# Kernel optimization log

Hardware: AMD Instinct MI355X
Metric: run time of the kernel (lower is better)

The kernel has to match this reference:

```python
import jax, jax.numpy as jnp
import numpy as np

TEMPERATURE = 0.5
BN_EPS = 1e-5
L2_EPS = 1e-12

B, D_IN, D_HID, D_OUT = 4096, 192, 512, 128


def setup_inputs() -> dict:
    key = jax.random.key(0)
    ks = jax.random.split(key, 4)
    return {
        "h1": jax.random.normal(ks[0], (B, D_IN), dtype=jnp.float32),
        "h2": jax.random.normal(ks[1], (B, D_IN), dtype=jnp.float32),
        "W1": jax.random.normal(ks[2], (D_HID, D_IN), dtype=jnp.float32) * (1.0 / np.sqrt(D_IN)),
        "b1": jnp.zeros((D_HID,), dtype=jnp.float32),
        "gamma": jnp.ones((D_HID,), dtype=jnp.float32),
        "beta": jnp.zeros((D_HID,), dtype=jnp.float32),
        "W2": jax.random.normal(ks[3], (D_OUT, D_HID), dtype=jnp.float32) * (1.0 / np.sqrt(D_HID)),
        "b2": jnp.zeros((D_OUT,), dtype=jnp.float32),
    }


def _projection_head(h, W1, b1, gamma, beta, W2, b2):
    # Linear -> BatchNorm1d (training-mode batch stats) -> ReLU -> Linear
    y = h @ W1.T + b1  # (B, D_HID)
    mean = jnp.mean(y, axis=0)
    var = jnp.mean((y - mean) ** 2, axis=0)  # biased var, as torch BN uses for normalization
    y = (y - mean) * jax.lax.rsqrt(var + BN_EPS) * gamma + beta
    y = jax.nn.relu(y)
    return y @ W2.T + b2  # (B, D_OUT)


def _l2_normalize(z):
    n = jnp.sqrt(jnp.sum(z * z, axis=1, keepdims=True))
    return z / jnp.maximum(n, L2_EPS)


def reference(h1, h2, W1, b1, gamma, beta, W2, b2):
    z1 = _l2_normalize(_projection_head(h1, W1, b1, gamma, beta, W2, b2))
    z2 = _l2_normalize(_projection_head(h2, W1, b1, gamma, beta, W2, b2))

    # NT-Xent, fully vectorized (equivalent to the per-row torch loop):
    z = jnp.concatenate([z1, z2], axis=0)            # (2B, D)
    sim = (z @ z.T) / TEMPERATURE                    # (2B, 2B)
    n2 = z.shape[0]
    sim = jnp.where(jnp.eye(n2, dtype=bool), -jnp.inf, sim)
    # positive pair similarity: sim[i, i+B] and sim[i+B, i] == z1_i . z2_i / T
    pos = jnp.sum(z1 * z2, axis=1) / TEMPERATURE     # (B,)
    pos = jnp.concatenate([pos, pos])                # (2B,)
    # excluding index i from the row equals including it since diag is -inf
    lse = jax.nn.logsumexp(sim, axis=1)              # (2B,)
    loss = jnp.mean(lse - pos)
    return loss, z1, z2
```

## Files before the change

### kernel.cpp

```cpp
#include <hip/hip_runtime.h>


#define NB   4096
#define DIN  192
#define DHID 512
#define DOUT 128
#define N2   8192
#define NSPLIT 32
#define SIM_ITERS 16

typedef short short8 __attribute__((ext_vector_type(8)));
typedef float floatx4 __attribute__((ext_vector_type(4)));

__device__ inline float fast_exp2(float x) {
#if __has_builtin(__builtin_amdgcn_exp2f)
    return __builtin_amdgcn_exp2f(x);
#else
    return exp2f(x);
#endif
}

__device__ inline unsigned short bf16_rne(float x) {
    unsigned int u = __float_as_uint(x);
    return (unsigned short)((u + 0x7fffu + ((u >> 16) & 1u)) >> 16);
}

#define NW1 (DHID * DIN / 4)
#define NW2 (DOUT * DHID / 4)
#define NH  (NB * DIN / 4)
__global__ __launch_bounds__(256) void convert_w(
    const float* __restrict__ W1, const float* __restrict__ W2,
    const float* __restrict__ h1, const float* __restrict__ h2,
    unsigned short* __restrict__ W1b, unsigned short* __restrict__ W2b,
    unsigned short* __restrict__ Hb)
{
    int id = blockIdx.x * 256 + threadIdx.x;
    const float* src; unsigned short* dst; int off;
    if (id < NW1)                 { src = W1; dst = W1b; off = id; }
    else if (id < NW1 + NW2)      { src = W2; dst = W2b; off = id - NW1; }
    else if (id < NW1 + NW2 + NH) { src = h1; dst = Hb;  off = id - NW1 - NW2; }
    else if (id < NW1 + NW2 + 2 * NH) {
        src = h2; dst = Hb + (size_t)NB * DIN; off = id - NW1 - NW2 - NH;
    } else return;
    float4 x = ((const float4*)src)[off];
    unsigned int p0 = bf16_rne(x.x) | ((unsigned int)bf16_rne(x.y) << 16);
    unsigned int p1 = bf16_rne(x.z) | ((unsigned int)bf16_rne(x.w) << 16);
    ((uint2*)dst)[off] = make_uint2(p0, p1);
}

__global__ __launch_bounds__(256) void gemm1_mfma(
    const unsigned short* __restrict__ Hb,
    const unsigned short* __restrict__ W1b, const float* __restrict__ b1,
    unsigned short* __restrict__ Ybf,
    float* __restrict__ psumc, float* __restrict__ psqc)
{
    const int t = threadIdx.x;
    const int wave = t >> 6, lane = t & 63;
    const int quad = lane >> 4, l15 = lane & 15;
    const int mb = blockIdx.x;
    const int m0 = mb * 64 + wave * 16;
    const int n0 = blockIdx.y * 64;
    const int v  = (mb >= 64);

    short8 a[6];
    {
        const short8* ap = (const short8*)(Hb + (size_t)(m0 + l15) * DIN + quad * 8);
        #pragma unroll
        for (int kc = 0; kc < 6; ++kc) a[kc] = ap[kc * 4];
    }

    #pragma unroll
    for (int nt = 0; nt < 4; ++nt) {
        const int col = n0 + nt * 16 + l15;
        const short8* bptr = (const short8*)(W1b + (size_t)col * DIN + quad * 8);
        short8 b[6];
        #pragma unroll
        for (int kc = 0; kc < 6; ++kc) b[kc] = bptr[kc * 4];
        floatx4 acc = {0.f,0.f,0.f,0.f};
        #pragma unroll
        for (int kc = 0; kc < 6; ++kc)
            acc = __builtin_amdgcn_mfma_f32_16x16x32_bf16(a[kc], b[kc], acc, 0,0,0);
        const float bias = b1[col];
        float cs = 0.f, cq = 0.f;
        #pragma unroll
        for (int reg = 0; reg < 4; ++reg) {
            float y = acc[reg] + bias;
            int row = m0 + quad * 4 + reg;
            Ybf[(size_t)row * DHID + col] = bf16_rne(y);
            cs += y; cq += y * y;
        }
        cs += __shfl_xor(cs, 16); cs += __shfl_xor(cs, 32);
        cq += __shfl_xor(cq, 16); cq += __shfl_xor(cq, 32);
        if (quad == 0) {
            atomicAdd(psumc + v * DHID + col, cs);
            atomicAdd(psqc  + v * DHID + col, cq);
        }
    }
}

#define ZSCALE 1.6986436f

__global__ __launch_bounds__(512) void gemm2_mfma(
    const unsigned short* __restrict__ Ybf, const unsigned short* __restrict__ W2b,
    const float* __restrict__ psumc, const float* __restrict__ psqc,
    const float* __restrict__ gamma, const float* __restrict__ beta,
    const float* __restrict__ b2,
    unsigned short* __restrict__ Zb, float* __restrict__ outz)
{
    __shared__ float sc_sh[DHID], sh_sh[DHID];
    __shared__ float sq_lds[8][16];
    const int t = threadIdx.x;
    const int wave = t >> 6, lane = t & 63;
    const int quad = lane >> 4, l15 = lane & 15;
    const int mtbase = blockIdx.x * 16;
    const int v = (mtbase >= NB);
    const int col = wave * 16 + l15;

    {
        int c = t;
        float mean = psumc[v * DHID + c] * (1.0f / NB);
        float var  = psqc [v * DHID + c] * (1.0f / NB) - mean * mean;
        float rstd = rsqrtf(var + 1e-5f);
        float scv = gamma[c] * rstd;
        sc_sh[c] = scv;
        sh_sh[c] = beta[c] - mean * scv;
    }
    __syncthreads();

    const unsigned short* yrow = Ybf + (size_t)(mtbase + l15) * DHID + quad * 8;
    const unsigned short* wcol = W2b + (size_t)col * DHID + quad * 8;

    uint4 ycur = *(const uint4*)yrow;
    short8 bcur = *(const short8*)wcol;
    floatx4 acc = {0.f, 0.f, 0.f, 0.f};

    for (int kc = 0; kc < 16; ++kc) {
        uint4 ynext; short8 bnext;
        const int kn = (kc + 1) & 15;
        ynext = *(const uint4*)(yrow + kn * 32);
        bnext = *(const short8*)(wcol + kn * 32);

        const int k = kc * 32 + quad * 8;
        const float4 s0 = *(const float4*)&sc_sh[k], s1 = *(const float4*)&sc_sh[k + 4];
        const float4 h0 = *(const float4*)&sh_sh[k], h1v = *(const float4*)&sh_sh[k + 4];
        const unsigned int yw[4] = {ycur.x, ycur.y, ycur.z, ycur.w};
        float xs[8];
        #pragma unroll
        for (int c2 = 0; c2 < 4; ++c2) {
            xs[c2 * 2]     = __uint_as_float(yw[c2] << 16);
            xs[c2 * 2 + 1] = __uint_as_float(yw[c2] & 0xffff0000u);
        }
        const float ss[8] = {s0.x,s0.y,s0.z,s0.w,s1.x,s1.y,s1.z,s1.w};
        const float hh[8] = {h0.x,h0.y,h0.z,h0.w,h1v.x,h1v.y,h1v.z,h1v.w};
        short8 afr;
        #pragma unroll
        for (int j = 0; j < 8; ++j)
            afr[j] = (short)bf16_rne(fmaxf(xs[j] * ss[j] + hh[j], 0.f));
        acc = __builtin_amdgcn_mfma_f32_16x16x32_bf16(afr, bcur, acc, 0,0,0);
        ycur = ynext; bcur = bnext;
    }

    const float bias = b2[col];
    float zv[4];
    #pragma unroll
    for (int reg = 0; reg < 4; ++reg) {
        zv[reg] = acc[reg] + bias;
        float q = zv[reg] * zv[reg];
        q += __shfl_xor(q, 1); q += __shfl_xor(q, 2);
        q += __shfl_xor(q, 4); q += __shfl_xor(q, 8);
        if (l15 == 0) sq_lds[wave][quad * 4 + reg] = q;
    }
    __syncthreads();
    #pragma unroll
    for (int reg = 0; reg < 4; ++reg) {
        float tot = 0.f;
        #pragma unroll
        for (int w = 0; w < 8; ++w) tot += sq_lds[w][quad * 4 + reg];
        float inv = 1.0f / fmaxf(sqrtf(tot), 1e-12f);
        const int row = mtbase + quad * 4 + reg;
        float z = zv[reg] * inv;
        outz[(size_t)row * DOUT + col] = z;
        Zb[(size_t)row * DOUT + col] = bf16_rne(z * ZSCALE);
    }
}

__global__ __launch_bounds__(256) void sim_mfma(
    const unsigned short* __restrict__ Zb, float* __restrict__ psum)
{
    const int t = threadIdx.x;
    const int wave = t >> 6, lane = t & 63;
    const int quad = lane >> 4, l15 = lane & 15;
    const int mbase = blockIdx.x * 256 + wave * 64;
    const int cs = blockIdx.y;
    const int cbase = cs * (N2 / NSPLIT);

    short8 a[4][4];
    #pragma unroll
    for (int at = 0; at < 4; ++at) {
        const short8* zra = (const short8*)(Zb + (size_t)(mbase + at * 16 + l15) * DOUT + quad * 8);
        #pragma unroll
        for (int kc = 0; kc < 4; ++kc) a[at][kc] = zra[kc * 4];
    }

    float rs[4][4];
    #pragma unroll
    for (int at = 0; at < 4; ++at)
        #pragma unroll
        for (int r = 0; r < 4; ++r) rs[at][r] = 0.f;

    short8 bcur[4], bnext[4];
    {
        const short8* zb = (const short8*)(Zb + (size_t)(cbase + l15) * DOUT + quad * 8);
        #pragma unroll
        for (int kc = 0; kc < 4; ++kc) bcur[kc] = zb[kc * 4];
    }

    for (int nt = 0; nt < SIM_ITERS; ++nt) {
        const int cn = cbase + ((nt + 1) & (SIM_ITERS - 1)) * 16;
        const short8* zbn = (const short8*)(Zb + (size_t)(cn + l15) * DOUT + quad * 8);
        #pragma unroll
        for (int kc = 0; kc < 4; ++kc) bnext[kc] = zbn[kc * 4];

        floatx4 acc[4] = {{0.f,0.f,0.f,0.f},{0.f,0.f,0.f,0.f},
                          {0.f,0.f,0.f,0.f},{0.f,0.f,0.f,0.f}};
        #pragma unroll
        for (int kc = 0; kc < 4; ++kc)
            #pragma unroll
            for (int at = 0; at < 4; ++at)
                acc[at] = __builtin_amdgcn_mfma_f32_16x16x32_bf16(a[at][kc], bcur[kc], acc[at], 0, 0, 0);

        #pragma unroll
        for (int at = 0; at < 4; ++at)
            #pragma unroll
            for (int r = 0; r < 4; ++r)
                rs[at][r] += fast_exp2(acc[at][r]);

        #pragma unroll
        for (int kc = 0; kc < 4; ++kc) bcur[kc] = bnext[kc];
    }

    #pragma unroll
    for (int at = 0; at < 4; ++at) {
        const int gi0 = mbase + at * 16 + quad * 4;
        #pragma unroll
        for (int r = 0; r < 4; ++r) {
            float s = rs[at][r];
            s += __shfl_xor(s, 1);
            s += __shfl_xor(s, 2);
            s += __shfl_xor(s, 4);
            s += __shfl_xor(s, 8);
            if (l15 == 0) psum[(size_t)cs * N2 + gi0 + r] = s;
        }
    }
}

__global__ __launch_bounds__(256) void row_finalize(
    const unsigned short* __restrict__ Zb, const float* __restrict__ psum,
    float* __restrict__ out)
{
    int i = blockIdx.x * 256 + threadIdx.x;
    float s = 0.f;
    for (int cs = 0; cs < NSPLIT; ++cs) s += psum[(size_t)cs * N2 + i];
    int k = i & (NB - 1);
    const uint4* z1 = (const uint4*)(Zb + (size_t)k * DOUT);
    const uint4* z2 = (const uint4*)(Zb + (size_t)(k + NB) * DOUT);
    float d12 = 0.f, d11 = 0.f, d22 = 0.f;
    #pragma unroll
    for (int q = 0; q < 16; ++q) {
        uint4 a = z1[q], bqq = z2[q];
        const unsigned int aw[4] = {a.x, a.y, a.z, a.w};
        const unsigned int bw[4] = {bqq.x, bqq.y, bqq.z, bqq.w};
        #pragma unroll
        for (int c = 0; c < 4; ++c) {
            float alo = __uint_as_float(aw[c] << 16);
            float ahi = __uint_as_float(aw[c] & 0xffff0000u);
            float blo = __uint_as_float(bw[c] << 16);
            float bhi = __uint_as_float(bw[c] & 0xffff0000u);
            d12 += alo * blo + ahi * bhi;
            d11 += alo * alo + ahi * ahi;
            d22 += blo * blo + bhi * bhi;
        }
    }
    float dself = (i < NB) ? d11 : d22;
    float rowval = logf(s - fast_exp2(dself)) - d12 * 0.69314718f;

    float r = rowval;
    r += __shfl_xor(r, 1);  r += __shfl_xor(r, 2);  r += __shfl_xor(r, 4);
    r += __shfl_xor(r, 8);  r += __shfl_xor(r, 16); r += __shfl_xor(r, 32);
    __shared__ float wsr[4];
    int lane = threadIdx.x & 63, w = threadIdx.x >> 6;
    if (lane == 0) wsr[w] = r;
    __syncthreads();
    if (threadIdx.x == 0)
        atomicAdd(out, (wsr[0] + wsr[1] + wsr[2] + wsr[3]) * (1.0f / N2));
}

extern "C" void kernel_launch(void* const* d_in, const int* in_sizes, int n_in,
                              void* d_out, int out_size, void* d_ws, size_t ws_size,
                              hipStream_t stream)
{
    const float* h1    = (const float*)d_in[0];
    const float* h2    = (const float*)d_in[1];
    const float* W1    = (const float*)d_in[2];
    const float* b1    = (const float*)d_in[3];
    const float* gamma = (const float*)d_in[4];
    const float* beta  = (const float*)d_in[5];
    const float* W2    = (const float*)d_in[6];
    const float* b2    = (const float*)d_in[7];
    float* out = (float*)d_out;

    float* ws      = (float*)d_ws;
    float* psumc   = ws;
    float* psqc    = psumc + 1024;
    unsigned short* W1b = (unsigned short*)(psqc + 1024);
    unsigned short* W2b = W1b + DHID * DIN;
    unsigned short* Hb  = (unsigned short*)(W2b + DOUT * DHID);
    unsigned short* Ybf = Hb + (size_t)N2 * DIN;
    float* psum    = (float*)(Ybf + (size_t)N2 * DHID);
    unsigned short* Zb = (unsigned short*)(psum + (size_t)NSPLIT * N2);

    hipMemsetAsync(psumc, 0, 2048 * sizeof(float), stream);
    hipMemsetAsync(out, 0, sizeof(float), stream);

    const int conv_blocks = (NW1 + NW2 + 2 * NH + 255) / 256;
    convert_w   <<<dim3(conv_blocks),  256, 0, stream>>>(W1, W2, h1, h2, W1b, W2b, Hb);
    gemm1_mfma  <<<dim3(128, 8),       256, 0, stream>>>(Hb, W1b, b1, Ybf, psumc, psqc);
    gemm2_mfma  <<<dim3(512),          512, 0, stream>>>(Ybf, W2b, psumc, psqc, gamma, beta, b2, Zb, out + 1);
    sim_mfma    <<<dim3(32, NSPLIT),   256, 0, stream>>>(Zb, psum);
    row_finalize<<<dim3(32),           256, 0, stream>>>(Zb, psum, out);
}
```

Before: 166.3 us.

## Fuse input bf16 conversion into gemm1 and double sim split count

Stops converting h1/h2 to bf16 in a separate pass and instead loads the fp32 rows inside gemm1 and rounds them to bf16 in registers. This removes a write and reread of the intermediate bf16 activation buffer. The similarity kernel now splits columns 64 ways with 8 iterations each, which gives more blocks but makes the row finalize reduce over more partials. Unroll-1 pragmas are added to the gemm2 and sim loops. gemm1 now reads fp32 data, which is twice as many bytes and is duplicated across the 8 column blocks.

```diff
diff --git a/kernel.cpp b/kernel.cpp
--- a/kernel.cpp
+++ b/kernel.cpp
@@ -6,8 +6,8 @@
 #define DHID 512
 #define DOUT 128
 #define N2   8192
-#define NSPLIT 32
-#define SIM_ITERS 16
+#define NSPLIT 64
+#define SIM_ITERS 8
 
 typedef short short8 __attribute__((ext_vector_type(8)));
 typedef float floatx4 __attribute__((ext_vector_type(4)));
@@ -25,23 +25,17 @@
     return (unsigned short)((u + 0x7fffu + ((u >> 16) & 1u)) >> 16);
 }
 
-#define NW1 (DHID * DIN / 4)
-#define NW2 (DOUT * DHID / 4)
-#define NH  (NB * DIN / 4)
 __global__ __launch_bounds__(256) void convert_w(
     const float* __restrict__ W1, const float* __restrict__ W2,
-    const float* __restrict__ h1, const float* __restrict__ h2,
-    unsigned short* __restrict__ W1b, unsigned short* __restrict__ W2b,
-    unsigned short* __restrict__ Hb)
-{
+    unsigned short* __restrict__ W1b, unsigned short* __restrict__ W2b)
+{
+    const int NW1 = DHID * DIN / 4;
+    const int NW2 = DOUT * DHID / 4;
     int id = blockIdx.x * 256 + threadIdx.x;
     const float* src; unsigned short* dst; int off;
-    if (id < NW1)                 { src = W1; dst = W1b; off = id; }
-    else if (id < NW1 + NW2)      { src = W2; dst = W2b; off = id - NW1; }
-    else if (id < NW1 + NW2 + NH) { src = h1; dst = Hb;  off = id - NW1 - NW2; }
-    else if (id < NW1 + NW2 + 2 * NH) {
-        src = h2; dst = Hb + (size_t)NB * DIN; off = id - NW1 - NW2 - NH;
-    } else return;
+    if (id < NW1)            { src = W1; dst = W1b; off = id; }
+    else if (id < NW1 + NW2) { src = W2; dst = W2b; off = id - NW1; }
+    else return;
     float4 x = ((const float4*)src)[off];
     unsigned int p0 = bf16_rne(x.x) | ((unsigned int)bf16_rne(x.y) << 16);
     unsigned int p1 = bf16_rne(x.z) | ((unsigned int)bf16_rne(x.w) << 16);
@@ -49,7 +43,7 @@
 }
 
 __global__ __launch_bounds__(256) void gemm1_mfma(
-    const unsigned short* __restrict__ Hb,
+    const float* __restrict__ h1, const float* __restrict__ h2,
     const unsigned short* __restrict__ W1b, const float* __restrict__ b1,
     unsigned short* __restrict__ Ybf,
     float* __restrict__ psumc, float* __restrict__ psqc)
@@ -64,9 +58,17 @@
 
     short8 a[6];
     {
-        const short8* ap = (const short8*)(Hb + (size_t)(m0 + l15) * DIN + quad * 8);
-        #pragma unroll
-        for (int kc = 0; kc < 6; ++kc) a[kc] = ap[kc * 4];
+        int row = m0 + l15;
+        const float* hsrc = (row < NB) ? (h1 + (size_t)row * DIN)
+                                       : (h2 + (size_t)(row - NB) * DIN);
+        #pragma unroll
+        for (int kc = 0; kc < 6; ++kc) {
+            const float4* p = (const float4*)(hsrc + kc * 32 + quad * 8);
+            float4 x0 = p[0], x1 = p[1];
+            float xs[8] = {x0.x,x0.y,x0.z,x0.w,x1.x,x1.y,x1.z,x1.w};
+            #pragma unroll
+            for (int j = 0; j < 8; ++j) a[kc][j] = (short)bf16_rne(xs[j]);
+        }
     }
 
     #pragma unroll
@@ -134,11 +136,11 @@
     short8 bcur = *(const short8*)wcol;
     floatx4 acc = {0.f, 0.f, 0.f, 0.f};
 
+    #pragma unroll 1
     for (int kc = 0; kc < 16; ++kc) {
-        uint4 ynext; short8 bnext;
         const int kn = (kc + 1) & 15;
-        ynext = *(const uint4*)(yrow + kn * 32);
-        bnext = *(const short8*)(wcol + kn * 32);
+        uint4 ynext = *(const uint4*)(yrow + kn * 32);
+        short8 bnext = *(const short8*)(wcol + kn * 32);
 
         const int k = kc * 32 + quad * 8;
         const float4 s0 = *(const float4*)&sc_sh[k], s1 = *(const float4*)&sc_sh[k + 4];
@@ -215,6 +217,7 @@
         for (int kc = 0; kc < 4; ++kc) bcur[kc] = zb[kc * 4];
     }
 
+    #pragma unroll 1
     for (int nt = 0; nt < SIM_ITERS; ++nt) {
         const int cn = cbase + ((nt + 1) & (SIM_ITERS - 1)) * 16;
         const short8* zbn = (const short8*)(Zb + (size_t)(cn + l15) * DOUT + quad * 8);
@@ -314,18 +317,16 @@
     float* psqc    = psumc + 1024;
     unsigned short* W1b = (unsigned short*)(psqc + 1024);
     unsigned short* W2b = W1b + DHID * DIN;
-    unsigned short* Hb  = (unsigned short*)(W2b + DOUT * DHID);
-    unsigned short* Ybf = Hb + (size_t)N2 * DIN;
+    unsigned short* Ybf = W2b + DOUT * DHID;
     float* psum    = (float*)(Ybf + (size_t)N2 * DHID);
     unsigned short* Zb = (unsigned short*)(psum + (size_t)NSPLIT * N2);
 
     hipMemsetAsync(psumc, 0, 2048 * sizeof(float), stream);
     hipMemsetAsync(out, 0, sizeof(float), stream);
 
-    const int conv_blocks = (NW1 + NW2 + 2 * NH + 255) / 256;
-    convert_w   <<<dim3(conv_blocks),  256, 0, stream>>>(W1, W2, h1, h2, W1b, W2b, Hb);
-    gemm1_mfma  <<<dim3(128, 8),       256, 0, stream>>>(Hb, W1b, b1, Ybf, psumc, psqc);
-    gemm2_mfma  <<<dim3(512),          512, 0, stream>>>(Ybf, W2b, psumc, psqc, gamma, beta, b2, Zb, out + 1);
-    sim_mfma    <<<dim3(32, NSPLIT),   256, 0, stream>>>(Zb, psum);
-    row_finalize<<<dim3(32),           256, 0, stream>>>(Zb, psum, out);
-}
+    convert_w   <<<dim3(160),        256, 0, stream>>>(W1, W2, W1b, W2b);
+    gemm1_mfma  <<<dim3(128, 8),     256, 0, stream>>>(h1, h2, W1b, b1, Ybf, psumc, psqc);
+    gemm2_mfma  <<<dim3(512),        512, 0, stream>>>(Ybf, W2b, psumc, psqc, gamma, beta, b2, Zb, out + 1);
+    sim_mfma    <<<dim3(32, NSPLIT), 256, 0, stream>>>(Zb, psum);
+    row_finalize<<<dim3(32),         256, 0, stream>>>(Zb, psum, out);
+}
```

After: 179.3 us. 1.08x slower.
